# Performance work log

Hardware: AMD Instinct MI355X
Metric: run time of the kernel (lower is better)

Reference implementation:

```python
import jax, jax.numpy as jnp
import numpy as np

D = 1024
H = 16
DH = D // H  # 64
EPS = 1e-6


def setup_inputs() -> dict:
    key = jax.random.key(0)
    ks = jax.random.split(key, 12)
    B, Nq, Nk = 4, 2048, 2048
    s = 1.0 / np.sqrt(D)
    return {
        "x": jax.random.normal(ks[0], (B, Nq, D), dtype=jnp.float32),
        "context": jax.random.normal(ks[1], (B, Nk, D), dtype=jnp.float32),
        "Wq": jax.random.normal(ks[2], (D, D), dtype=jnp.float32) * s,
        "bq": jnp.zeros((D,), dtype=jnp.float32),
        "Wk": jax.random.normal(ks[3], (D, D), dtype=jnp.float32) * s,
        "bk": jnp.zeros((D,), dtype=jnp.float32),
        "Wv": jax.random.normal(ks[4], (D, D), dtype=jnp.float32) * s,
        "bv": jnp.zeros((D,), dtype=jnp.float32),
        "Wo": jax.random.normal(ks[5], (D, D), dtype=jnp.float32) * s,
        "bo": jnp.zeros((D,), dtype=jnp.float32),
    }


def _split_heads(t):
    B, N, _ = t.shape
    return t.reshape(B, N, H, DH).transpose(0, 2, 1, 3)  # (B,H,N,DH)


def reference(x, context, Wq, bq, Wk, bk, Wv, bv, Wo, bo):
    B, Nq, _ = x.shape
    # QKV projections (torch Linear: x @ W.T + b)
    q = _split_heads(x @ Wq.T + bq)          # (B,H,Nq,DH)
    k = _split_heads(context @ Wk.T + bk)    # (B,H,Nk,DH)
    v = _split_heads(context @ Wv.T + bv)    # (B,H,Nk,DH)
    # QK-norm (use_qk_norm=True), scale buffer = 1.0
    q = q / (jnp.linalg.norm(q, axis=-1, keepdims=True) + EPS)
    k = k / (jnp.linalg.norm(k, axis=-1, keepdims=True) + EPS)
    scale = jnp.float32(1.0)
    attn = jnp.einsum("bhqd,bhkd->bhqk", q, k) * scale
    attn = jax.nn.softmax(attn, axis=-1)
    out = jnp.einsum("bhqk,bhkd->bhqd", attn, v)  # (B,H,Nq,DH)
    out = out.transpose(0, 2, 1, 3).reshape(B, Nq, D)
    return out @ Wo.T + bo
```

## Files before the change

### kernel.cpp

```cpp
#include <hip/hip_runtime.h>

typedef unsigned short u16;
typedef unsigned int u32;
typedef __attribute__((ext_vector_type(8))) short bf16x8;
typedef __attribute__((ext_vector_type(4))) float f32x4;
typedef __attribute__((ext_vector_type(16))) float f32x16;
typedef __attribute__((ext_vector_type(4))) u32 u32x4;

#define D_MODEL 1024
#define NHEAD 16
#define DHEAD 64
#define SEQ 2048
#define BATCH 4
#define MTOT (BATCH * SEQ)
#define LOG2E 1.4426950408889634f

#define MFMA16(A, B, C) __builtin_amdgcn_mfma_f32_16x16x32_bf16((A), (B), (C), 0, 0, 0)
#define MFMA32(A, B, C) __builtin_amdgcn_mfma_f32_32x32x16_bf16((A), (B), (C), 0, 0, 0)

__device__ __forceinline__ u16 f2bf(float f) {
  u32 u = __builtin_bit_cast(u32, f);
  u = (u + 0x7FFFu + ((u >> 16) & 1u)) >> 16;
  return (u16)u;
}

__device__ __forceinline__ void async_copy16(void* lds, const void* g) {
  __builtin_amdgcn_global_load_lds(
      (const __attribute__((address_space(1))) u32*)g,
      (__attribute__((address_space(3))) u32*)lds, 16, 0, 0);
}

__device__ __forceinline__ u32 cvtpk_bf16(float lo, float hi) {
  u32 r;
  asm("v_cvt_pk_bf16_f32 %0, %1, %2" : "=v"(r) : "v"(lo), "v"(hi));
  return r;
}
__device__ __forceinline__ void permswap(u32& a, u32& b) {
  asm("v_permlane32_swap_b32 %0, %1" : "+v"(a), "+v"(b));
}

__device__ __forceinline__ void wg_barrier() {
  __builtin_amdgcn_sched_barrier(0);
  asm volatile("s_barrier" ::: "memory");
  __builtin_amdgcn_sched_barrier(0);
}
#define VMCNT(N) asm volatile("s_waitcnt vmcnt(" #N ")" ::: "memory")

__global__ void cvt_all(const float* __restrict__ x, const float* __restrict__ ctx,
                        const float* __restrict__ Wq, const float* __restrict__ Wk,
                        const float* __restrict__ Wv, const float* __restrict__ Wo,
                        u16* __restrict__ xb, u16* __restrict__ cb,
                        u16* __restrict__ wqb, u16* __restrict__ wkb,
                        u16* __restrict__ wvb, u16* __restrict__ wob) {
  const int NX = 1 << 21;
  const int NW = 1 << 18;
  const int total = 2 * NX + 4 * NW;
  int i = blockIdx.x * blockDim.x + threadIdx.x;
  const int st = gridDim.x * blockDim.x;
  for (; i < total; i += st) {
    const float* s; u16* d; int j;
    if (i < NX)            { s = x;   d = xb;  j = i; }
    else if (i < 2 * NX)   { s = ctx; d = cb;  j = i - NX; }
    else {
      int k = i - 2 * NX;
      int wi = k >> 18;
      j = k & (NW - 1);
      s = (wi == 0) ? Wq : (wi == 1) ? Wk : (wi == 2) ? Wv : Wo;
      d = (wi == 0) ? wqb : (wi == 1) ? wkb : (wi == 2) ? wvb : wob;
    }
    float4 v = ((const float4*)s)[j];
    ushort4 o;
    o.x = f2bf(v.x); o.y = f2bf(v.y); o.z = f2bf(v.z); o.w = f2bf(v.w);
    ((ushort4*)d)[j] = o;
  }
}

__global__ __launch_bounds__(256, 3) void gemm_qkv(
    const u16* __restrict__ xb, const u16* __restrict__ cb,
    const u16* __restrict__ wqb, const u16* __restrict__ wkvb,
    const float* __restrict__ bq, const float* __restrict__ bk,
    const float* __restrict__ bv,
    u16* __restrict__ Qb, u16* __restrict__ Kb, u16* __restrict__ Vtb) {
  __shared__ u16 As[128 * 64];
  __shared__ u16 Bs[128 * 64];
  const int K = 1024;
  const int tid = threadIdx.x;
  const int l = tid & 63;
  const int wid = tid >> 6;
  const int bid = blockIdx.x;
  const int swz = (bid & 7) * 192 + (bid >> 3);
  const bool isQ = swz < 512;
  const u16* A;
  const u16* Bw;
  int m0, n0;
  if (isQ) {
    A = xb; Bw = wqb;
    m0 = (swz >> 3) * 128;
    n0 = (swz & 7) * 128;
  } else {
    const int s = swz - 512;
    A = cb; Bw = wkvb;
    m0 = (s >> 4) * 128;
    n0 = (s & 15) * 128;
  }
  const int wr = wid >> 1, wc = wid & 1;
  const int r = l & 15, kg = l >> 4;
  f32x4 acc[4][4] = {};
  char* AsB = (char*)As;
  char* BsB = (char*)Bs;
  const int arow = l >> 3;
  const int agran = (l & 7) ^ arow;

  for (int kt = 0; kt < K; kt += 64) {
#pragma unroll
    for (int cc = 0; cc < 4; ++cc) {
      int c = wid + (cc << 2);
      int rowi = (c << 3) + arow;
      const char* ga = (const char*)A + ((size_t)(m0 + rowi) * K + kt) * 2 + agran * 16;
      async_copy16(AsB + c * 1024, ga);
      const char* gb = (const char*)Bw + ((size_t)(n0 + rowi) * K + kt) * 2 + agran * 16;
      async_copy16(BsB + c * 1024, gb);
    }
    __syncthreads();
#pragma unroll
    for (int half = 0; half < 2; ++half) {
      const int g = ((half << 2) + kg) ^ (r & 7);
      bf16x8 af[4], bf[4];
#pragma unroll
      for (int i = 0; i < 4; ++i) {
        af[i] = *(const bf16x8*)(AsB + (wr * 64 + i * 16 + r) * 128 + g * 16);
        bf[i] = *(const bf16x8*)(BsB + (wc * 64 + i * 16 + r) * 128 + g * 16);
      }
#pragma unroll
      for (int i = 0; i < 4; ++i)
#pragma unroll
        for (int j = 0; j < 4; ++j)
          acc[i][j] = MFMA16(af[i], bf[j], acc[i][j]);
    }
    __syncthreads();
  }

  const int colbase = n0 + wc * 64;
  const bool isV = (!isQ) && (colbase >= 1024);
  if (!isV) {
    u16* C = isQ ? Qb : Kb;
    const float* bias = isQ ? bq : bk;
    const float sMul = isQ ? LOG2E : 1.0f;
    float bvj[4];
#pragma unroll
    for (int j = 0; j < 4; ++j) bvj[j] = bias[colbase + j * 16 + r];
#pragma unroll
    for (int i = 0; i < 4; ++i) {
      const int row0 = m0 + wr * 64 + i * 16 + kg * 4;
#pragma unroll
      for (int jj = 0; jj < 4; ++jj) {
        float t[4];
        float s2 = 0.f;
#pragma unroll
        for (int j = 0; j < 4; ++j) {
          t[j] = acc[i][j][jj] + bvj[j];
          s2 += t[j] * t[j];
        }
        s2 += __shfl_xor(s2, 1);
        s2 += __shfl_xor(s2, 2);
        s2 += __shfl_xor(s2, 4);
        s2 += __shfl_xor(s2, 8);
        const float inv = sMul / (sqrtf(s2) + 1e-6f);
#pragma unroll
        for (int j = 0; j < 4; ++j)
          C[(size_t)(row0 + jj) * D_MODEL + colbase + j * 16 + r] = f2bf(t[j] * inv);
      }
    }
  } else {
#pragma unroll
    for (int i = 0; i < 4; ++i) {
#pragma unroll
      for (int j = 0; j < 4; ++j) {
        const int col = colbase + j * 16 + r;
        const float bvv = bv[col - 1024];
        const int row0 = m0 + wr * 64 + i * 16 + kg * 4;
        const int hh = (col - 1024) >> 6, dh = col & 63;
        const int bb = row0 >> 11, tok = row0 & 2047;
        ushort4 o;
        o.x = f2bf(acc[i][j][0] + bvv);
        o.y = f2bf(acc[i][j][1] + bvv);
        o.z = f2bf(acc[i][j][2] + bvv);
        o.w = f2bf(acc[i][j][3] + bvv);
        *(ushort4*)(Vtb + ((size_t)((bb * 16 + hh) * 64 + dh) * SEQ + tok)) = o;
      }
    }
  }
}

__global__ __launch_bounds__(256, 3) void gemm_out(const u16* __restrict__ A,
                                                   const u16* __restrict__ Bw,
                                                   const float* __restrict__ bias,
                                                   float* __restrict__ Cout) {
  __shared__ u16 As[128 * 64];
  __shared__ u16 Bs[128 * 64];
  const int K = 1024, N = 1024;
  const int tid = threadIdx.x;
  const int l = tid & 63;
  const int wid = tid >> 6;
  const int bid = blockIdx.x;
  const int swz = (bid & 7) * 64 + (bid >> 3);
  const int m0 = (swz >> 3) * 128;
  const int n0 = (swz & 7) * 128;
  const int wr = wid >> 1, wc = wid & 1;
  const int r = l & 15, kg = l >> 4;
  f32x4 acc[4][4] = {};
  char* AsB = (char*)As;
  char* BsB = (char*)Bs;
  const int arow = l >> 3;
  const int agran = (l & 7) ^ arow;

  for (int kt = 0; kt < K; kt += 64) {
#pragma unroll
    for (int cc = 0; cc < 4; ++cc) {
      int c = wid + (cc << 2);
      int rowi = (c << 3) + arow;
      const char* ga = (const char*)A + ((size_t)(m0 + rowi) * K + kt) * 2 + agran * 16;
      async_copy16(AsB + c * 1024, ga);
      const char* gb = (const char*)Bw + ((size_t)(n0 + rowi) * K + kt) * 2 + agran * 16;
      async_copy16(BsB + c * 1024, gb);
    }
    __syncthreads();
#pragma unroll
    for (int half = 0; half < 2; ++half) {
      const int g = ((half << 2) + kg) ^ (r & 7);
      bf16x8 af[4], bf[4];
#pragma unroll
      for (int i = 0; i < 4; ++i) {
        af[i] = *(const bf16x8*)(AsB + (wr * 64 + i * 16 + r) * 128 + g * 16);
        bf[i] = *(const bf16x8*)(BsB + (wc * 64 + i * 16 + r) * 128 + g * 16);
      }
#pragma unroll
      for (int i = 0; i < 4; ++i)
#pragma unroll
        for (int j = 0; j < 4; ++j)
          acc[i][j] = MFMA16(af[i], bf[j], acc[i][j]);
    }
    __syncthreads();
  }
#pragma unroll
  for (int i = 0; i < 4; ++i) {
#pragma unroll
    for (int j = 0; j < 4; ++j) {
      const int col = n0 + wc * 64 + j * 16 + r;
      const float bvv = bias[col];
      const int row0 = m0 + wr * 64 + i * 16 + kg * 4;
#pragma unroll
      for (int jj = 0; jj < 4; ++jj)
        Cout[(size_t)(row0 + jj) * N + col] = acc[i][j][jj] + bvv;
    }
  }
}

#define KVB 64
#define NT (SEQ / KVB)

__global__ __launch_bounds__(256, 4) void attn_kernel(const u16* __restrict__ Q,
                                                      const u16* __restrict__ K,
                                                      const u16* __restrict__ Vt,
                                                      u16* __restrict__ O) {
  __shared__ alignas(16) u16 Ks[2][KVB * 64];
  __shared__ alignas(16) u16 Vs[2][64 * KVB];
  const int tid = threadIdx.x;
  const int l = tid & 63;
  const int wid = tid >> 6;
  const int qg = l & 31;
  const int half = l >> 5;
  const int bid = blockIdx.x;
  const int swz = (bid & 7) * 128 + (bid >> 3);
  const int qt = swz & 15;
  const int bh = swz >> 4;
  const int b = bh >> 4, h = bh & 15;

  const int srow = l >> 3, slot = l & 7;
  const int r0 = (wid << 3) + srow;
  const int r1 = ((wid + 4) << 3) + srow;
  const int sw0 = (r0 ^ (r0 >> 3)) & 7;
  const int sw1 = (r1 ^ (r1 >> 3)) & 7;
  const u16* pK0 = K + ((size_t)(b * SEQ) + r0) * D_MODEL + h * 64 + (slot ^ sw0) * 8;
  const u16* pK1 = K + ((size_t)(b * SEQ) + r1) * D_MODEL + h * 64 + (slot ^ sw1) * 8;
  const u16* pV0 = Vt + ((size_t)(bh * 64) + r0) * SEQ + (slot ^ sw0) * 8;
  const u16* pV1 = Vt + ((size_t)(bh * 64) + r1) * SEQ + (slot ^ sw1) * 8;
  const int ldsc0 = wid * 1024, ldsc1 = (wid + 4) * 1024;

  bf16x8 qf[4];
  {
    const u16* q0 = Q + ((size_t)(b * SEQ + qt * 128 + wid * 32 + qg)) * D_MODEL + h * 64 + half * 8;
#pragma unroll
    for (int dc = 0; dc < 4; ++dc) qf[dc] = *(const bf16x8*)(q0 + dc * 16);
  }

  int koff[2][4], voff[2][2][2];
#pragma unroll
  for (int t32 = 0; t32 < 2; ++t32) {
    const int rowK = t32 * 32 + qg;
    const int swk = (rowK ^ (rowK >> 3)) & 7;
#pragma unroll
    for (int dc = 0; dc < 4; ++dc)
      koff[t32][dc] = rowK * 128 + (((dc * 2 + half) ^ swk) << 4);
#pragma unroll
    for (int cc = 0; cc < 2; ++cc) {
      const int qw = ((t32 * 2 + cc) << 1) + half;
#pragma unroll
      for (int dt = 0; dt < 2; ++dt) {
        const int rowV = dt * 32 + qg;
        voff[t32][cc][dt] = rowV * 128 + ((qw ^ ((rowV ^ (rowV >> 3)) & 7)) << 4);
      }
    }
  }

  f32x16 oacc[2] = {};
  float lrun = 0.f;

  auto stage = [&](int bufi) {
    char* KsX = (char*)Ks[bufi];
    char* VsX = (char*)Vs[bufi];
    async_copy16(KsX + ldsc0, pK0);
    async_copy16(KsX + ldsc1, pK1);
    async_copy16(VsX + ldsc0, pV0);
    async_copy16(VsX + ldsc1, pV1);
    pK0 += (size_t)KVB * D_MODEL;
    pK1 += (size_t)KVB * D_MODEL;
    pV0 += KVB;
    pV1 += KVB;
  };

  auto process = [&](const char* KsC, const char* VsC) {
    f32x16 st[2] = {};
    __builtin_amdgcn_s_setprio(1);
#pragma unroll
    for (int t32 = 0; t32 < 2; ++t32)
#pragma unroll
      for (int dc = 0; dc < 4; ++dc) {
        bf16x8 kf = *(const bf16x8*)(KsC + koff[t32][dc]);
        st[t32] = MFMA32(kf, qf[dc], st[t32]);
      }
    __builtin_amdgcn_s_setprio(0);

    float rs0 = 0.f, rs1 = 0.f, rs2 = 0.f, rs3 = 0.f;
#pragma unroll
    for (int t32 = 0; t32 < 2; ++t32)
#pragma unroll
      for (int rr = 0; rr < 16; rr += 4) {
        float p0 = __builtin_amdgcn_exp2f(st[t32][rr + 0]);
        float p1 = __builtin_amdgcn_exp2f(st[t32][rr + 1]);
        float p2 = __builtin_amdgcn_exp2f(st[t32][rr + 2]);
        float p3 = __builtin_amdgcn_exp2f(st[t32][rr + 3]);
        st[t32][rr + 0] = p0; st[t32][rr + 1] = p1;
        st[t32][rr + 2] = p2; st[t32][rr + 3] = p3;
        rs0 += p0; rs1 += p1; rs2 += p2; rs3 += p3;
      }
    lrun += (rs0 + rs1) + (rs2 + rs3);

#pragma unroll
    for (int t32 = 0; t32 < 2; ++t32) {
#pragma unroll
      for (int cc = 0; cc < 2; ++cc) {
        const int base = cc * 8;
        u32 wA = cvtpk_bf16(st[t32][base + 0], st[t32][base + 1]);
        u32 wB = cvtpk_bf16(st[t32][base + 2], st[t32][base + 3]);
        u32 wC = cvtpk_bf16(st[t32][base + 4], st[t32][base + 5]);
        u32 wD = cvtpk_bf16(st[t32][base + 6], st[t32][base + 7]);
        permswap(wA, wC);
        permswap(wB, wD);
        u32x4 pw = {wA, wB, wC, wD};
        bf16x8 pf = __builtin_bit_cast(bf16x8, pw);
        __builtin_amdgcn_s_setprio(1);
#pragma unroll
        for (int dt = 0; dt < 2; ++dt) {
          bf16x8 vf = *(const bf16x8*)(VsC + voff[t32][cc][dt]);
          oacc[dt] = MFMA32(vf, pf, oacc[dt]);
        }
        __builtin_amdgcn_s_setprio(0);
      }
    }
  };

  stage(0);
  stage(1);
  VMCNT(0);
  wg_barrier();

  for (int tp = 0; tp < NT / 2 - 1; ++tp) {
    VMCNT(4);
    wg_barrier();
    process((const char*)Ks[0], (const char*)Vs[0]);
    wg_barrier();
    stage(0);
    VMCNT(4);
    wg_barrier();
    process((const char*)Ks[1], (const char*)Vs[1]);
    wg_barrier();
    stage(1);
  }
  VMCNT(4);
  wg_barrier();
  process((const char*)Ks[0], (const char*)Vs[0]);
  wg_barrier();
  VMCNT(0);
  wg_barrier();
  process((const char*)Ks[1], (const char*)Vs[1]);

  lrun += __shfl_xor(lrun, 32);
  const float inv = 1.0f / lrun;
  u32* orow = (u32*)(O + ((size_t)(b * SEQ + qt * 128 + wid * 32 + qg)) * D_MODEL + h * 64);
#pragma unroll
  for (int dt = 0; dt < 2; ++dt)
#pragma unroll
    for (int w = 0; w < 8; ++w) {
      const int dh = dt * 32 + (w & 1) * 2 + 8 * (w >> 1) + 4 * half;
      u32 pk = cvtpk_bf16(oacc[dt][2 * w] * inv, oacc[dt][2 * w + 1] * inv);
      orow[dh >> 1] = pk;
    }
}

extern "C" void kernel_launch(void* const* d_in, const int* in_sizes, int n_in,
                              void* d_out, int out_size, void* d_ws, size_t ws_size,
                              hipStream_t stream) {
  const float* x   = (const float*)d_in[0];
  const float* ctx = (const float*)d_in[1];
  const float* Wq  = (const float*)d_in[2];
  const float* bq  = (const float*)d_in[3];
  const float* Wk  = (const float*)d_in[4];
  const float* bk  = (const float*)d_in[5];
  const float* Wv  = (const float*)d_in[6];
  const float* bv  = (const float*)d_in[7];
  const float* Wo  = (const float*)d_in[8];
  const float* bo  = (const float*)d_in[9];
  float* out = (float*)d_out;

  const size_t NTOK = (size_t)MTOT * D_MODEL;
  const size_t WSZ = (size_t)D_MODEL * D_MODEL;
  u16* xb  = (u16*)d_ws;
  u16* cb  = xb + NTOK;
  u16* wqb = cb + NTOK;
  u16* wkb = wqb + WSZ;
  u16* wvb = wkb + WSZ;
  u16* wob = wvb + WSZ;
  u16* Qb  = wob + WSZ;
  u16* Kb  = Qb + NTOK;
  u16* Vtb = Kb + NTOK;
  (void)in_sizes; (void)n_in; (void)out_size; (void)ws_size;

  dim3 blk(256);
  cvt_all<<<2048, blk, 0, stream>>>(x, ctx, Wq, Wk, Wv, Wo, xb, cb, wqb, wkb, wvb, wob);

  gemm_qkv<<<1536, blk, 0, stream>>>(xb, cb, wqb, wkb, bq, bk, bv, Qb, Kb, Vtb);

  attn_kernel<<<1024, blk, 0, stream>>>(Qb, Kb, Vtb, xb);

  gemm_out<<<512, blk, 0, stream>>>(xb, wob, bo, out);
}
```

Baseline: 177.4 us.

## Replace QKV and output GEMMs with 8-wave triple-buffered pipelined template

Both projection GEMMs move to a single templated kernel that uses 512 threads, 256x128 tiles and a three-stage LDS ring. Global-to-LDS copies for the next-but-one tile are split into four parts and interleaved with four MFMA sub-phases, using explicit vmcnt/lgkmcnt waits, barriers and setprio to overlap loads with compute. The aim is to hide memory latency and reduce the per-iteration barrier stalls of the old single-buffered loop. In exchange there are more barriers per K-step, a larger LDS footprint and fewer blocks per grid, which may cut occupancy and load balance.

```diff
diff --git a/kernel.cpp b/kernel.cpp
--- a/kernel.cpp
+++ b/kernel.cpp
@@ -45,6 +45,7 @@
   __builtin_amdgcn_sched_barrier(0);
 }
 #define VMCNT(N) asm volatile("s_waitcnt vmcnt(" #N ")" ::: "memory")
+#define LGKM0()  do { asm volatile("s_waitcnt lgkmcnt(0)" ::: "memory"); __builtin_amdgcn_sched_barrier(0); } while (0)
 
 __global__ void cvt_all(const float* __restrict__ x, const float* __restrict__ ctx,
                         const float* __restrict__ Wq, const float* __restrict__ Wk,
@@ -75,71 +76,149 @@
   }
 }
 
-__global__ __launch_bounds__(256, 3) void gemm_qkv(
+#define BM8 256
+#define BN8 128
+#define BK8 64
+#define GK 1024
+#define NIT (GK / BK8)
+#define ABYTES (BM8 * BK8 * 2)
+#define BUFB (ABYTES + BN8 * BK8 * 2)
+
+template <int MODE>
+__global__ __launch_bounds__(512, 2) void gemm8p(
     const u16* __restrict__ xb, const u16* __restrict__ cb,
     const u16* __restrict__ wqb, const u16* __restrict__ wkvb,
     const float* __restrict__ bq, const float* __restrict__ bk,
-    const float* __restrict__ bv,
-    u16* __restrict__ Qb, u16* __restrict__ Kb, u16* __restrict__ Vtb) {
-  __shared__ u16 As[128 * 64];
-  __shared__ u16 Bs[128 * 64];
-  const int K = 1024;
+    const float* __restrict__ bvv,
+    u16* __restrict__ Qb, u16* __restrict__ Kb, u16* __restrict__ Vtb,
+    float* __restrict__ fout) {
+  __shared__ alignas(16) char ldsbuf[3 * BUFB];
   const int tid = threadIdx.x;
   const int l = tid & 63;
   const int wid = tid >> 6;
   const int bid = blockIdx.x;
-  const int swz = (bid & 7) * 192 + (bid >> 3);
-  const bool isQ = swz < 512;
-  const u16* A;
-  const u16* Bw;
+  const u16 *A, *Bw;
   int m0, n0;
-  if (isQ) {
+  bool isQ = false;
+  if (MODE == 0) {
+    const int swz = (bid & 7) * 96 + (bid >> 3);
+    isQ = swz < 256;
+    if (isQ) { A = xb; Bw = wqb; m0 = (swz >> 3) * BM8; n0 = (swz & 7) * BN8; }
+    else { const int s = swz - 256; A = cb; Bw = wkvb; m0 = (s >> 4) * BM8; n0 = (s & 15) * BN8; }
+  } else {
+    const int swz = (bid & 7) * 32 + (bid >> 3);
     A = xb; Bw = wqb;
-    m0 = (swz >> 3) * 128;
-    n0 = (swz & 7) * 128;
-  } else {
-    const int s = swz - 512;
-    A = cb; Bw = wkvb;
-    m0 = (s >> 4) * 128;
-    n0 = (s & 15) * 128;
+    m0 = (swz >> 3) * BM8; n0 = (swz & 7) * BN8;
   }
   const int wr = wid >> 1, wc = wid & 1;
   const int r = l & 15, kg = l >> 4;
+  const int arow8 = l >> 3;
+  const int agran = (l & 7) ^ arow8;
+
+  const u16* pA0 = A + (size_t)(m0 + (wid + 0) * 8 + arow8) * GK + agran * 8;
+  const u16* pA1 = A + (size_t)(m0 + (wid + 8) * 8 + arow8) * GK + agran * 8;
+  const u16* pA2 = A + (size_t)(m0 + (wid + 16) * 8 + arow8) * GK + agran * 8;
+  const u16* pA3 = A + (size_t)(m0 + (wid + 24) * 8 + arow8) * GK + agran * 8;
+  const u16* pB0 = Bw + (size_t)(n0 + (wid + 0) * 8 + arow8) * GK + agran * 8;
+  const u16* pB1 = Bw + (size_t)(n0 + (wid + 8) * 8 + arow8) * GK + agran * 8;
+
   f32x4 acc[4][4] = {};
-  char* AsB = (char*)As;
-  char* BsB = (char*)Bs;
-  const int arow = l >> 3;
-  const int agran = (l & 7) ^ arow;
-
-  for (int kt = 0; kt < K; kt += 64) {
-#pragma unroll
-    for (int cc = 0; cc < 4; ++cc) {
-      int c = wid + (cc << 2);
-      int rowi = (c << 3) + arow;
-      const char* ga = (const char*)A + ((size_t)(m0 + rowi) * K + kt) * 2 + agran * 16;
-      async_copy16(AsB + c * 1024, ga);
-      const char* gb = (const char*)Bw + ((size_t)(n0 + rowi) * K + kt) * 2 + agran * 16;
-      async_copy16(BsB + c * 1024, gb);
-    }
-    __syncthreads();
-#pragma unroll
-    for (int half = 0; half < 2; ++half) {
-      const int g = ((half << 2) + kg) ^ (r & 7);
-      bf16x8 af[4], bf[4];
-#pragma unroll
-      for (int i = 0; i < 4; ++i) {
-        af[i] = *(const bf16x8*)(AsB + (wr * 64 + i * 16 + r) * 128 + g * 16);
-        bf[i] = *(const bf16x8*)(BsB + (wc * 64 + i * 16 + r) * 128 + g * 16);
-      }
-#pragma unroll
-      for (int i = 0; i < 4; ++i)
-#pragma unroll
-        for (int j = 0; j < 4; ++j)
-          acc[i][j] = MFMA16(af[i], bf[j], acc[i][j]);
-    }
-    __syncthreads();
-  }
-
+
+  auto stage_part = [&](char* base, int p) {
+    if (p == 0) {
+      async_copy16(base + (wid + 0) * 1024, pA0);
+      async_copy16(base + (wid + 8) * 1024, pA1);
+    } else if (p == 1) {
+      async_copy16(base + (wid + 16) * 1024, pA2);
+      async_copy16(base + (wid + 24) * 1024, pA3);
+    } else if (p == 2) {
+      async_copy16(base + ABYTES + (wid + 0) * 1024, pB0);
+    } else {
+      async_copy16(base + ABYTES + (wid + 8) * 1024, pB1);
+      pA0 += 64; pA1 += 64; pA2 += 64; pA3 += 64; pB0 += 64; pB1 += 64;
+    }
+  };
+
+  auto phase = [&](const char* rb, int ih, int jh, char* sb, int sp, bool ds, int vm) {
+    const char* Ab = rb;
+    const char* Bb = rb + ABYTES;
+    bf16x8 af[2][2], bf[2][2];
+#pragma unroll
+    for (int ii = 0; ii < 2; ++ii) {
+      const int rowA = wr * 64 + (ih * 2 + ii) * 16 + r;
+#pragma unroll
+      for (int hf = 0; hf < 2; ++hf) {
+        const int g = ((hf << 2) + kg) ^ (r & 7);
+        af[ii][hf] = *(const bf16x8*)(Ab + rowA * 128 + g * 16);
+      }
+    }
+#pragma unroll
+    for (int jj = 0; jj < 2; ++jj) {
+      const int rowB = wc * 64 + (jh * 2 + jj) * 16 + r;
+#pragma unroll
+      for (int hf = 0; hf < 2; ++hf) {
+        const int g = ((hf << 2) + kg) ^ (r & 7);
+        bf[jj][hf] = *(const bf16x8*)(Bb + rowB * 128 + g * 16);
+      }
+    }
+    if (ds) stage_part(sb, sp);
+    wg_barrier();
+    LGKM0();
+    __builtin_amdgcn_s_setprio(1);
+#pragma unroll
+    for (int hf = 0; hf < 2; ++hf)
+#pragma unroll
+      for (int ii = 0; ii < 2; ++ii)
+#pragma unroll
+        for (int jj = 0; jj < 2; ++jj)
+          acc[ih * 2 + ii][jh * 2 + jj] =
+              MFMA16(af[ii][hf], bf[jj][hf], acc[ih * 2 + ii][jh * 2 + jj]);
+    __builtin_amdgcn_s_setprio(0);
+    if (vm == 1) { VMCNT(6); }
+    else if (vm == 2) { VMCNT(0); }
+    wg_barrier();
+  };
+
+  char* b0 = ldsbuf;
+  char* b1 = ldsbuf + BUFB;
+  char* b2 = ldsbuf + 2 * BUFB;
+
+#pragma unroll
+  for (int p = 0; p < 4; ++p) stage_part(b0, p);
+#pragma unroll
+  for (int p = 0; p < 4; ++p) stage_part(b1, p);
+  VMCNT(6);
+  wg_barrier();
+
+  int rm = 0;
+  for (int t = 0; t < NIT; ++t) {
+    char* rb = (rm == 0) ? b0 : (rm == 1) ? b1 : b2;
+    char* sb = (rm == 0) ? b2 : (rm == 1) ? b0 : b1;
+    const bool ds = (t + 2 < NIT);
+    const int vml = (t < NIT - 2) ? 1 : (t == NIT - 2) ? 2 : 0;
+    phase(rb, 0, 0, sb, 0, ds, 0);
+    phase(rb, 0, 1, sb, 1, ds, 0);
+    phase(rb, 1, 0, sb, 2, ds, 0);
+    phase(rb, 1, 1, sb, 3, ds, vml);
+    rm = (rm == 2) ? 0 : rm + 1;
+  }
+
+  if (MODE == 1) {
+    const int N = 1024;
+#pragma unroll
+    for (int i = 0; i < 4; ++i) {
+#pragma unroll
+      for (int j = 0; j < 4; ++j) {
+        const int col = n0 + wc * 64 + j * 16 + r;
+        const float bb = bq[col];
+        const int row0 = m0 + wr * 64 + i * 16 + kg * 4;
+#pragma unroll
+        for (int jj = 0; jj < 4; ++jj)
+          fout[(size_t)(row0 + jj) * N + col] = acc[i][j][jj] + bb;
+      }
+    }
+    return;
+  }
   const int colbase = n0 + wc * 64;
   const bool isV = (!isQ) && (colbase >= 1024);
   if (!isV) {
@@ -154,12 +233,12 @@
       const int row0 = m0 + wr * 64 + i * 16 + kg * 4;
 #pragma unroll
       for (int jj = 0; jj < 4; ++jj) {
-        float t[4];
+        float tv[4];
         float s2 = 0.f;
 #pragma unroll
         for (int j = 0; j < 4; ++j) {
-          t[j] = acc[i][j][jj] + bvj[j];
-          s2 += t[j] * t[j];
+          tv[j] = acc[i][j][jj] + bvj[j];
+          s2 += tv[j] * tv[j];
         }
         s2 += __shfl_xor(s2, 1);
         s2 += __shfl_xor(s2, 2);
@@ -168,7 +247,7 @@
         const float inv = sMul / (sqrtf(s2) + 1e-6f);
 #pragma unroll
         for (int j = 0; j < 4; ++j)
-          C[(size_t)(row0 + jj) * D_MODEL + colbase + j * 16 + r] = f2bf(t[j] * inv);
+          C[(size_t)(row0 + jj) * D_MODEL + colbase + j * 16 + r] = f2bf(tv[j] * inv);
       }
     }
   } else {
@@ -177,81 +256,17 @@
 #pragma unroll
       for (int j = 0; j < 4; ++j) {
         const int col = colbase + j * 16 + r;
-        const float bvv = bv[col - 1024];
+        const float bb = bvv[col - 1024];
         const int row0 = m0 + wr * 64 + i * 16 + kg * 4;
         const int hh = (col - 1024) >> 6, dh = col & 63;
-        const int bb = row0 >> 11, tok = row0 & 2047;
+        const int bbk = row0 >> 11, tok = row0 & 2047;
         ushort4 o;
-        o.x = f2bf(acc[i][j][0] + bvv);
-        o.y = f2bf(acc[i][j][1] + bvv);
-        o.z = f2bf(acc[i][j][2] + bvv);
-        o.w = f2bf(acc[i][j][3] + bvv);
-        *(ushort4*)(Vtb + ((size_t)((bb * 16 + hh) * 64 + dh) * SEQ + tok)) = o;
-      }
-    }
-  }
-}
-
-__global__ __launch_bounds__(256, 3) void gemm_out(const u16* __restrict__ A,
-                                                   const u16* __restrict__ Bw,
-                                                   const float* __restrict__ bias,
-                                                   float* __restrict__ Cout) {
-  __shared__ u16 As[128 * 64];
-  __shared__ u16 Bs[128 * 64];
-  const int K = 1024, N = 1024;
-  const int tid = threadIdx.x;
-  const int l = tid & 63;
-  const int wid = tid >> 6;
-  const int bid = blockIdx.x;
-  const int swz = (bid & 7) * 64 + (bid >> 3);
-  const int m0 = (swz >> 3) * 128;
-  const int n0 = (swz & 7) * 128;
-  const int wr = wid >> 1, wc = wid & 1;
-  const int r = l & 15, kg = l >> 4;
-  f32x4 acc[4][4] = {};
-  char* AsB = (char*)As;
-  char* BsB = (char*)Bs;
-  const int arow = l >> 3;
-  const int agran = (l & 7) ^ arow;
-
-  for (int kt = 0; kt < K; kt += 64) {
-#pragma unroll
-    for (int cc = 0; cc < 4; ++cc) {
-      int c = wid + (cc << 2);
-      int rowi = (c << 3) + arow;
-      const char* ga = (const char*)A + ((size_t)(m0 + rowi) * K + kt) * 2 + agran * 16;
-      async_copy16(AsB + c * 1024, ga);
-      const char* gb = (const char*)Bw + ((size_t)(n0 + rowi) * K + kt) * 2 + agran * 16;
-      async_copy16(BsB + c * 1024, gb);
-    }
-    __syncthreads();
-#pragma unroll
-    for (int half = 0; half < 2; ++half) {
-      const int g = ((half << 2) + kg) ^ (r & 7);
-      bf16x8 af[4], bf[4];
-#pragma unroll
-      for (int i = 0; i < 4; ++i) {
-        af[i] = *(const bf16x8*)(AsB + (wr * 64 + i * 16 + r) * 128 + g * 16);
-        bf[i] = *(const bf16x8*)(BsB + (wc * 64 + i * 16 + r) * 128 + g * 16);
-      }
-#pragma unroll
-      for (int i = 0; i < 4; ++i)
-#pragma unroll
-        for (int j = 0; j < 4; ++j)
-          acc[i][j] = MFMA16(af[i], bf[j], acc[i][j]);
-    }
-    __syncthreads();
-  }
-#pragma unroll
-  for (int i = 0; i < 4; ++i) {
-#pragma unroll
-    for (int j = 0; j < 4; ++j) {
-      const int col = n0 + wc * 64 + j * 16 + r;
-      const float bvv = bias[col];
-      const int row0 = m0 + wr * 64 + i * 16 + kg * 4;
-#pragma unroll
-      for (int jj = 0; jj < 4; ++jj)
-        Cout[(size_t)(row0 + jj) * N + col] = acc[i][j][jj] + bvv;
+        o.x = f2bf(acc[i][j][0] + bb);
+        o.y = f2bf(acc[i][j][1] + bb);
+        o.z = f2bf(acc[i][j][2] + bb);
+        o.w = f2bf(acc[i][j][3] + bb);
+        *(ushort4*)(Vtb + ((size_t)((bbk * 16 + hh) * 64 + dh) * SEQ + tok)) = o;
+      }
     }
   }
 }
@@ -446,12 +461,12 @@
   u16* Vtb = Kb + NTOK;
   (void)in_sizes; (void)n_in; (void)out_size; (void)ws_size;
 
-  dim3 blk(256);
-  cvt_all<<<2048, blk, 0, stream>>>(x, ctx, Wq, Wk, Wv, Wo, xb, cb, wqb, wkb, wvb, wob);
-
-  gemm_qkv<<<1536, blk, 0, stream>>>(xb, cb, wqb, wkb, bq, bk, bv, Qb, Kb, Vtb);
-
-  attn_kernel<<<1024, blk, 0, stream>>>(Qb, Kb, Vtb, xb);
-
-  gemm_out<<<512, blk, 0, stream>>>(xb, wob, bo, out);
-}
+  cvt_all<<<2048, 256, 0, stream>>>(x, ctx, Wq, Wk, Wv, Wo, xb, cb, wqb, wkb, wvb, wob);
+
+  gemm8p<0><<<768, 512, 0, stream>>>(xb, cb, wqb, wkb, bq, bk, bv, Qb, Kb, Vtb, nullptr);
+
+  attn_kernel<<<1024, 256, 0, stream>>>(Qb, Kb, Vtb, xb);
+
+  gemm8p<1><<<256, 512, 0, stream>>>(xb, nullptr, wob, nullptr, bo, nullptr, nullptr,
+                                     nullptr, nullptr, nullptr, out);
+}
```

New measurement: 198.0 us. 1.12x slower.
